# Performance work log

Measured on AMD Instinct MI355X. Metric: run time of the kernel, lower is better.

Reference implementation:

```python
import jax, jax.numpy as jnp
import numpy as np

B, N, C = 8192, 4, 1024
H = 16
D = C // H              # head_dim = 64
P = 4                   # proj_dim (Linformer reduced length)
IDX_I, IDX_J = 1, 2     # Return_attn_way(use_cls=True, attn_selet_way=0)
SCALE = D ** -0.5


def setup_inputs() -> dict:
    key = jax.random.key(0)
    ks = jax.random.split(key, 6)
    std = 0.02
    x = jax.random.normal(ks[0], (B, N, C), dtype=jnp.float32)
    W_qkv = jax.random.normal(ks[1], (C, 3 * C), dtype=jnp.float32) * std   # qkv_bias=False
    W_proj = jax.random.normal(ks[2], (C, C), dtype=jnp.float32) * std
    b_proj = jnp.zeros((C,), dtype=jnp.float32)
    W_E = jax.random.normal(ks[3], (P, N), dtype=jnp.float32) * std         # torch Linear weight [out,in]
    W_F = jax.random.normal(ks[4], (P, N), dtype=jnp.float32) * std
    return {"x": x, "W_qkv": W_qkv, "W_proj": W_proj, "b_proj": b_proj,
            "W_E": W_E, "W_F": W_F}


def reference(x, W_qkv, W_proj, b_proj, W_E, W_F):
    b, n, c = x.shape
    # qkv projection -> [B,N,3,H,D] -> q,k,v each [B,H,N,D]
    qkv = (x @ W_qkv).reshape(b, n, 3, H, D)
    qkv = jnp.transpose(qkv, (2, 0, 3, 1, 4))
    q, k, v = qkv[0], qkv[1], qkv[2]
    q = q * SCALE  # q_norm/k_norm are Identity (qk_norm=False)

    # gathered single-token score: q[:,:,IDX_I,:] @ k[:,:,IDX_J,:].T -> [B,H,H]
    # (torch transpose(-2,-1) on the [B,H,D] slice swaps H and D)
    attn_sel = jnp.einsum('bhd,bgd->bhg', q[:, :, IDX_I, :], k[:, :, IDX_J, :])
    attn_sel_sig = jax.nn.sigmoid(attn_sel)

    # Linformer E/F projection along the sequence axis: [B,H,N,D] -> [B,H,P,D]
    k_low = jnp.einsum('bhnd,pn->bhpd', k, W_E)
    v_low = jnp.einsum('bhnd,pn->bhpd', v, W_F)

    # reduced softmax attention: [B,H,N,P]
    attn = jnp.einsum('bhnd,bhpd->bhnp', q, k_low)
    attn = jax.nn.softmax(attn, axis=-1)  # attn_drop is identity (p=0, eval)
    out = jnp.einsum('bhnp,bhpd->bhnd', attn, v_low)

    # merge heads and output projection
    out = jnp.transpose(out, (0, 2, 1, 3)).reshape(b, n, c)
    out = out @ W_proj.T + b_proj  # proj_drop identity
    return (out, attn_sel_sig)
```

## Files before the change

kernel.cpp:

```cpp
#include <hip/hip_runtime.h>
#include <hip/hip_bf16.h>

#define B_   8192
#define C_   1024
#define H_   16
#define M_   (B_ * 4)
#define K_   1024
#define N1_  3072

typedef __attribute__((ext_vector_type(8))) short short8;
typedef __attribute__((ext_vector_type(4))) float f32x4;
typedef __attribute__((ext_vector_type(8))) int   int8v;

__device__ __forceinline__ unsigned short f2bf(float f) {
  union { float f; unsigned u; } v; v.f = f;
  unsigned r = v.u + 0x7fffu + ((v.u >> 16) & 1u);
  return (unsigned short)(r >> 16);
}
__device__ __forceinline__ float bf2f(unsigned short u) {
  union { unsigned u; float f; } v; v.u = ((unsigned)u) << 16;
  return v.f;
}
__device__ __forceinline__ int pk_fp8(float a, float b, float c, float d) {
  int r = __builtin_amdgcn_cvt_pk_fp8_f32(a, b, 0, false);
  r = __builtin_amdgcn_cvt_pk_fp8_f32(c, d, r, true);
  return r;
}

__global__ __launch_bounds__(256) void cast_x_k(const float* __restrict__ x,
                                                unsigned char* __restrict__ x8,
                                                unsigned short* __restrict__ xsel) {
  const int row = blockIdx.x;
  const int tid = threadIdx.x;
  float4 v = ((const float4*)(x + (size_t)row * 1024))[tid];
  ((int*)(x8 + (size_t)row * 1024))[tid] = pk_fp8(v.x, v.y, v.z, v.w);
  const int n = row & 3;
  if (n == 1 || n == 2) {
    ushort4 o;
    o.x = f2bf(v.x); o.y = f2bf(v.y); o.z = f2bf(v.z); o.w = f2bf(v.w);
    ((ushort4*)(xsel + ((size_t)(n - 1) * 8192 + (row >> 2)) * 1024))[tid] = o;
  }
}

__global__ __launch_bounds__(256) void transpose_wqkv_k(const float* __restrict__ in,
                                                        unsigned short* __restrict__ outb,
                                                        unsigned char* __restrict__ out8) {
  __shared__ float t[32][33];
  int tx = threadIdx.x, ty = threadIdx.y;
  int j0 = blockIdx.x * 32, c0 = blockIdx.y * 32;
#pragma unroll
  for (int i = 0; i < 4; ++i)
    t[ty + i * 8][tx] = in[(size_t)(c0 + ty + i * 8) * N1_ + j0 + tx];
  __syncthreads();
#pragma unroll
  for (int i = 0; i < 4; ++i) {
    int j = j0 + ty + i * 8;
    float v = t[tx][ty + i * 8];
    if (j < 1024) v *= 0.125f;
    outb[(size_t)j * K_ + c0 + tx] = f2bf(v);
    out8[(size_t)j * K_ + c0 + tx] =
        (unsigned char)(__builtin_amdgcn_cvt_pk_fp8_f32(v * 32.f, v * 32.f, 0, false) & 0xff);
  }
}

__global__ __launch_bounds__(256) void cast_wproj_k(const float* __restrict__ in,
                                                    unsigned char* __restrict__ out) {
  int i = blockIdx.x * 256 + threadIdx.x;
  float4 v = ((const float4*)in)[i];
  ((int*)out)[i] = pk_fp8(v.x * 32.f, v.y * 32.f, v.z * 32.f, v.w * 32.f);
}

__global__ __launch_bounds__(256) void gemm_fixup(const unsigned short* __restrict__ A,
                                                  const unsigned short* __restrict__ B0,
                                                  unsigned short* __restrict__ Cbf) {
  __shared__ unsigned short lsA[128 * 32];
  __shared__ unsigned short lsB[128 * 32];
  const int K = 1024, Ncols = 1024;
  const int tid = threadIdx.x;
  const int wave = tid >> 6, lane = tid & 63;
  const int wm = (wave >> 1) * 64, wn = (wave & 1) * 64;
  const long tile_m = (long)blockIdx.y * 128, tile_n = (long)blockIdx.x * 128;
  const unsigned short* Bm = B0 + (tile_m >= 8192 ? (size_t)1024 * 1024 : 0);

  f32x4 acc[4][4] = {};
  const int ci0 = (wave * 2 + 0) * 64 + lane;
  const int ci1 = (wave * 2 + 1) * 64 + lane;
  const int r0 = ci0 >> 2, kc0 = (ci0 & 3) * 8;
  const int r1 = ci1 >> 2, kc1 = (ci1 & 3) * 8;
  const unsigned short* gA0 = A + (tile_m + r0) * K + kc0;
  const unsigned short* gA1 = A + (tile_m + r1) * K + kc1;
  const unsigned short* gB0 = Bm + (tile_n + r0) * K + kc0;
  const unsigned short* gB1 = Bm + (tile_n + r1) * K + kc1;
  unsigned short* dA0 = lsA + (wave * 2 + 0) * 512;
  unsigned short* dA1 = lsA + (wave * 2 + 1) * 512;
  unsigned short* dB0 = lsB + (wave * 2 + 0) * 512;
  unsigned short* dB1 = lsB + (wave * 2 + 1) * 512;
  const int r16 = lane & 15, q8 = (lane >> 4) * 8;

  for (int kt = 0; kt < K; kt += 32) {
    __builtin_amdgcn_global_load_lds((const __attribute__((address_space(1))) void*)(gA0 + kt),
                                     (__attribute__((address_space(3))) void*)dA0, 16, 0, 0);
    __builtin_amdgcn_global_load_lds((const __attribute__((address_space(1))) void*)(gA1 + kt),
                                     (__attribute__((address_space(3))) void*)dA1, 16, 0, 0);
    __builtin_amdgcn_global_load_lds((const __attribute__((address_space(1))) void*)(gB0 + kt),
                                     (__attribute__((address_space(3))) void*)dB0, 16, 0, 0);
    __builtin_amdgcn_global_load_lds((const __attribute__((address_space(1))) void*)(gB1 + kt),
                                     (__attribute__((address_space(3))) void*)dB1, 16, 0, 0);
    __syncthreads();
    short8 afr[4], bfr[4];
#pragma unroll
    for (int mi = 0; mi < 4; ++mi)
      afr[mi] = *(const short8*)&lsA[(wm + mi * 16 + r16) * 32 + q8];
#pragma unroll
    for (int ni = 0; ni < 4; ++ni)
      bfr[ni] = *(const short8*)&lsB[(wn + ni * 16 + r16) * 32 + q8];
#pragma unroll
    for (int mi = 0; mi < 4; ++mi)
#pragma unroll
      for (int ni = 0; ni < 4; ++ni)
        acc[mi][ni] = __builtin_amdgcn_mfma_f32_16x16x32_bf16(afr[mi], bfr[ni], acc[mi][ni], 0, 0, 0);
    __syncthreads();
  }
  const int cl = lane & 15, rq = (lane >> 4) * 4;
#pragma unroll
  for (int mi = 0; mi < 4; ++mi)
#pragma unroll
    for (int ni = 0; ni < 4; ++ni) {
      long col = tile_n + wn + ni * 16 + cl;
#pragma unroll
      for (int r = 0; r < 4; ++r) {
        long row = tile_m + wm + mi * 16 + rq + r;
        Cbf[(size_t)row * Ncols + col] = f2bf(acc[mi][ni][r]);
      }
    }
}

template <int OUTMODE>
__global__ __launch_bounds__(512) void gemm_mx(const unsigned char* __restrict__ A,
                                               const unsigned char* __restrict__ Bm,
                                               unsigned short* __restrict__ Cbf,
                                               float* __restrict__ Cf,
                                               const float* __restrict__ bias,
                                               int K, int Ncols, int sA, int sB) {
  __shared__ unsigned char lds[131072];
  unsigned char* lsA0 = lds;
  unsigned char* lsB0 = lds + 32768;
  unsigned char* lsA1 = lds + 65536;
  unsigned char* lsB1 = lds + 98304;

  const int tid = threadIdx.x;
  const int wave = tid >> 6, lane = tid & 63;
  const int wm = (wave >> 2) * 128;
  const int wn = (wave & 3) * 64;
  const long tile_m = (long)blockIdx.y * 256, tile_n = (long)blockIdx.x * 256;

  f32x4 acc[8][4] = {};

  unsigned offA[4], offB[4];
#pragma unroll
  for (int j = 0; j < 4; ++j) {
    int ci = j * 512 + tid;
    int blk = ci >> 10, idb = ci & 1023;
    int qg = idb >> 8, id = idb & 255;
    int r2 = (id >> 3) & 1, r3 = (id >> 4) & 1;
    int rr0 = ((id >> 1) & 1) ^ r2, rr1 = ((id >> 2) & 1) ^ r3;
    int row = rr0 | (rr1 << 1) | (r2 << 2) | (r3 << 3) | ((id >> 5) << 4);
    int half = (id & 1) ^ rr0;
    offA[j] = (unsigned)((tile_m + blk * 128 + row) * K + qg * 32 + half * 16);
    offB[j] = (unsigned)((tile_n + blk * 128 + row) * K + qg * 32 + half * 16);
  }

  auto stage = [&](int kt, unsigned char* lA, unsigned char* lB) {
#pragma unroll
    for (int j = 0; j < 4; ++j)
      __builtin_amdgcn_global_load_lds(
          (const __attribute__((address_space(1))) void*)(A + offA[j] + kt),
          (__attribute__((address_space(3))) void*)(lA + j * 8192 + wave * 1024), 16, 0, 0);
#pragma unroll
    for (int j = 0; j < 4; ++j)
      __builtin_amdgcn_global_load_lds(
          (const __attribute__((address_space(1))) void*)(Bm + offB[j] + kt),
          (__attribute__((address_space(3))) void*)(lB + j * 8192 + wave * 1024), 16, 0, 0);
  };

  const int hl = lane & 15, qg = lane >> 4;
  const int swz = (hl & 12) << 3;
  const int laneFragBase = qg * 4096 + ((hl * 32) ^ swz) + ((hl & 1) << 4);
  const int Abase = (wm >> 7) * 16384 + laneFragBase;
  const int Bbase = (wn >> 7) * 16384 + (wn & 64) * 32 + laneFragBase;

  const int NT = K >> 7;
  stage(0, lsA0, lsB0);
  stage(128, lsA1, lsB1);
  asm volatile("s_waitcnt vmcnt(8)" ::: "memory");
  __builtin_amdgcn_s_barrier();

  for (int t = 0; t < NT; ++t) {
    unsigned char* lA = (t & 1) ? lsA1 : lsA0;
    unsigned char* lB = (t & 1) ? lsB1 : lsB0;

    int8v bfr[4];
#pragma unroll
    for (int ni = 0; ni < 4; ++ni) {
      int ad = Bbase + ni * 512;
      int4 h0 = *(const int4*)(lB + ad);
      int4 h1 = *(const int4*)(lB + (ad ^ 16));
      bfr[ni] = int8v{h0.x, h0.y, h0.z, h0.w, h1.x, h1.y, h1.z, h1.w};
    }
#pragma unroll
    for (int p = 0; p < 4; ++p) {
      int8v af[2];
#pragma unroll
      for (int mm = 0; mm < 2; ++mm) {
        int ad = Abase + (p * 2 + mm) * 512;
        int4 h0 = *(const int4*)(lA + ad);
        int4 h1 = *(const int4*)(lA + (ad ^ 16));
        af[mm] = int8v{h0.x, h0.y, h0.z, h0.w, h1.x, h1.y, h1.z, h1.w};
      }
      __builtin_amdgcn_s_barrier();
      asm volatile("s_waitcnt lgkmcnt(0)" ::: "memory");
      __builtin_amdgcn_s_setprio(1);
#pragma unroll
      for (int mm = 0; mm < 2; ++mm)
#pragma unroll
        for (int ni = 0; ni < 4; ++ni)
          acc[p * 2 + mm][ni] = __builtin_amdgcn_mfma_scale_f32_16x16x128_f8f6f4(
              af[mm], bfr[ni], acc[p * 2 + mm][ni], 0, 0, 0, sA, 0, sB);
      __builtin_amdgcn_s_setprio(0);
      __builtin_amdgcn_s_barrier();
    }
    if (t + 2 < NT) {
      stage((t + 2) << 7, lA, lB);
      asm volatile("s_waitcnt vmcnt(8)" ::: "memory");
      __builtin_amdgcn_s_barrier();
    } else if (t + 1 < NT) {
      asm volatile("s_waitcnt vmcnt(0)" ::: "memory");
      __builtin_amdgcn_s_barrier();
    }
  }

  const int cl = lane & 15, rq = (lane >> 4) * 4;
#pragma unroll
  for (int mi = 0; mi < 8; ++mi)
#pragma unroll
    for (int ni = 0; ni < 4; ++ni) {
      long col = tile_n + wn + ni * 16 + cl;
      float bv = (OUTMODE == 1) ? bias[col] : 0.f;
#pragma unroll
      for (int r = 0; r < 4; ++r) {
        long row = tile_m + wm + mi * 16 + rq + r;
        if (OUTMODE == 0)
          Cbf[(size_t)row * Ncols + col] = f2bf(acc[mi][ni][r]);
        else
          Cf[(size_t)row * Ncols + col] = acc[mi][ni][r] + bv;
      }
    }
}

__global__ __launch_bounds__(256) void attn_mfma_k(const unsigned short* __restrict__ qkv,
                                                   const unsigned short* __restrict__ q1,
                                                   const unsigned short* __restrict__ k2,
                                                   const float* __restrict__ WE,
                                                   const float* __restrict__ WF,
                                                   unsigned char* __restrict__ hmid8,
                                                   float* __restrict__ attn_sel) {
  __shared__ float As[4][16 * 17 + 2];
  const int tid = threadIdx.x;
  const int wave = tid >> 6, lane = tid & 63;
  const int b = blockIdx.x * 4 + wave;
  const size_t qb = (size_t)b * 4 * N1_;
  const int hl = lane & 15, qg = lane >> 4;

  f32x4 accS[4][4] = {};
  f32x4 accSel = {};
#pragma unroll
  for (int ch = 0; ch < 2; ++ch) {
    const int off = ch * 32 + qg * 8;
    short8 qf[4], kf[4];
#pragma unroll
    for (int n = 0; n < 4; ++n)
      qf[n] = *(const short8*)(qkv + qb + (size_t)n * N1_ + 0 + hl * 64 + off);
#pragma unroll
    for (int m = 0; m < 4; ++m)
      kf[m] = *(const short8*)(qkv + qb + (size_t)m * N1_ + 1024 + hl * 64 + off);
#pragma unroll
    for (int n = 0; n < 4; ++n)
#pragma unroll
      for (int m = 0; m < 4; ++m)
        accS[n][m] = __builtin_amdgcn_mfma_f32_16x16x32_bf16(qf[n], kf[m], accS[n][m], 0, 0, 0);
    short8 qs = *(const short8*)(q1 + (size_t)b * 1024 + hl * 64 + off);
    short8 ks = *(const short8*)(k2 + (size_t)b * 1024 + hl * 64 + off);
    accSel = __builtin_amdgcn_mfma_f32_16x16x32_bf16(qs, ks, accSel, 0, 0, 0);
  }

#pragma unroll
  for (int r = 0; r < 4; ++r)
    attn_sel[(size_t)b * 256 + (qg * 4 + r) * 16 + hl] = 1.f / (1.f + __expf(-accSel[r]));

  if ((hl >> 2) == qg) {
    const int h = hl, rr = h & 3;
    float Sm[4][4];
#pragma unroll
    for (int n = 0; n < 4; ++n)
#pragma unroll
      for (int m = 0; m < 4; ++m) Sm[n][m] = accS[n][m][rr];
#pragma unroll
    for (int n = 0; n < 4; ++n) {
      float lg[4];
#pragma unroll
      for (int p = 0; p < 4; ++p)
        lg[p] = Sm[n][0] * WE[p * 4] + Sm[n][1] * WE[p * 4 + 1] +
                Sm[n][2] * WE[p * 4 + 2] + Sm[n][3] * WE[p * 4 + 3];
      float mx = fmaxf(fmaxf(lg[0], lg[1]), fmaxf(lg[2], lg[3]));
      float e0 = __expf(lg[0] - mx), e1 = __expf(lg[1] - mx);
      float e2 = __expf(lg[2] - mx), e3 = __expf(lg[3] - mx);
      float inv = 1.f / (e0 + e1 + e2 + e3);
      e0 *= inv; e1 *= inv; e2 *= inv; e3 *= inv;
#pragma unroll
      for (int m = 0; m < 4; ++m)
        As[wave][h * 17 + n * 4 + m] =
            e0 * WF[0 * 4 + m] + e1 * WF[1 * 4 + m] + e2 * WF[2 * 4 + m] + e3 * WF[3 * 4 + m];
    }
  }
  __syncthreads();

  {
    const int h = lane & 15, dg = lane >> 4;
    float Ap[4][4];
#pragma unroll
    for (int n = 0; n < 4; ++n)
#pragma unroll
      for (int m = 0; m < 4; ++m) Ap[n][m] = As[wave][h * 17 + n * 4 + m];

    float outv[4][16] = {};
#pragma unroll
    for (int m = 0; m < 4; ++m) {
      const unsigned short* vp = qkv + qb + (size_t)m * N1_ + 2048 + h * 64 + dg * 16;
      short8 v0 = *(const short8*)(vp);
      short8 v1 = *(const short8*)(vp + 8);
      float vf[16];
#pragma unroll
      for (int j = 0; j < 8; ++j) {
        vf[j] = bf2f((unsigned short)v0[j]);
        vf[8 + j] = bf2f((unsigned short)v1[j]);
      }
#pragma unroll
      for (int n = 0; n < 4; ++n)
#pragma unroll
        for (int d = 0; d < 16; ++d) outv[n][d] += Ap[n][m] * vf[d];
    }
#pragma unroll
    for (int n = 0; n < 4; ++n) {
      int w0 = pk_fp8(outv[n][0] * 32.f, outv[n][1] * 32.f, outv[n][2] * 32.f, outv[n][3] * 32.f);
      int w1 = pk_fp8(outv[n][4] * 32.f, outv[n][5] * 32.f, outv[n][6] * 32.f, outv[n][7] * 32.f);
      int w2 = pk_fp8(outv[n][8] * 32.f, outv[n][9] * 32.f, outv[n][10] * 32.f, outv[n][11] * 32.f);
      int w3 = pk_fp8(outv[n][12] * 32.f, outv[n][13] * 32.f, outv[n][14] * 32.f, outv[n][15] * 32.f);
      *(int4*)(hmid8 + ((size_t)b * 4 + n) * 1024 + h * 64 + dg * 16) = make_int4(w0, w1, w2, w3);
    }
  }
}

extern "C" void kernel_launch(void* const* d_in, const int* in_sizes, int n_in,
                              void* d_out, int out_size, void* d_ws, size_t ws_size,
                              hipStream_t stream) {
  (void)in_sizes; (void)n_in; (void)out_size; (void)ws_size;
  const float* x      = (const float*)d_in[0];
  const float* W_qkv  = (const float*)d_in[1];
  const float* W_proj = (const float*)d_in[2];
  const float* b_proj = (const float*)d_in[3];
  const float* W_E    = (const float*)d_in[4];
  const float* W_F    = (const float*)d_in[5];

  float* out0 = (float*)d_out;
  float* out1 = out0 + (size_t)M_ * C_;

  char* ws = (char*)d_ws;
  unsigned short* xsel   = (unsigned short*)(ws);
  unsigned short* wqkvTb = (unsigned short*)(ws + 33554432);
  unsigned short* qkv_bf = (unsigned short*)(ws);
  unsigned char*  x8     = (unsigned char*)(ws + 201326592);
  unsigned char*  hmid8  = x8;
  unsigned char*  wqkvT8 = (unsigned char*)(ws + 234881024);
  unsigned char*  wproj8 = (unsigned char*)(ws + 238026752);
  unsigned short* q1k2   = (unsigned short*)(ws + 239075328);

  cast_x_k<<<32768, 256, 0, stream>>>(x, x8, xsel);
  transpose_wqkv_k<<<dim3(96, 32), dim3(32, 8), 0, stream>>>(W_qkv, wqkvTb, wqkvT8);
  cast_wproj_k<<<1024, 256, 0, stream>>>(W_proj, wproj8);

  gemm_fixup<<<dim3(8, 128), 256, 0, stream>>>(xsel, wqkvTb, q1k2);

  gemm_mx<0><<<dim3(12, 128), 512, 0, stream>>>(x8, wqkvT8, qkv_bf, nullptr, nullptr,
                                                1024, 3072, 127, 122);

  attn_mfma_k<<<B_ / 4, 256, 0, stream>>>(qkv_bf, q1k2, q1k2 + (size_t)8192 * 1024,
                                          W_E, W_F, hmid8, out1);

  gemm_mx<1><<<dim3(4, 128), 512, 0, stream>>>(hmid8, wproj8, nullptr, out0, b_proj,
                                               1024, 1024, 122, 122);
}
```

Baseline: 599.9 us.

## Restructure MX GEMM main loop with split prefetch and fewer barriers

Result: faster. 556.6 us (-7.2%).

```diff
diff --git a/kernel.cpp b/kernel.cpp
--- a/kernel.cpp
+++ b/kernel.cpp
@@ -143,10 +143,6 @@
                                                const float* __restrict__ bias,
                                                int K, int Ncols, int sA, int sB) {
   __shared__ unsigned char lds[131072];
-  unsigned char* lsA0 = lds;
-  unsigned char* lsB0 = lds + 32768;
-  unsigned char* lsA1 = lds + 65536;
-  unsigned char* lsB1 = lds + 98304;
 
   const int tid = threadIdx.x;
   const int wave = tid >> 6, lane = tid & 63;
@@ -170,73 +166,93 @@
     offB[j] = (unsigned)((tile_n + blk * 128 + row) * K + qg * 32 + half * 16);
   }
 
-  auto stage = [&](int kt, unsigned char* lA, unsigned char* lB) {
-#pragma unroll
-    for (int j = 0; j < 4; ++j)
-      __builtin_amdgcn_global_load_lds(
-          (const __attribute__((address_space(1))) void*)(A + offA[j] + kt),
-          (__attribute__((address_space(3))) void*)(lA + j * 8192 + wave * 1024), 16, 0, 0);
-#pragma unroll
-    for (int j = 0; j < 4; ++j)
-      __builtin_amdgcn_global_load_lds(
-          (const __attribute__((address_space(1))) void*)(Bm + offB[j] + kt),
-          (__attribute__((address_space(3))) void*)(lB + j * 8192 + wave * 1024), 16, 0, 0);
-  };
-
   const int hl = lane & 15, qg = lane >> 4;
   const int swz = (hl & 12) << 3;
   const int laneFragBase = qg * 4096 + ((hl * 32) ^ swz) + ((hl & 1) << 4);
   const int Abase = (wm >> 7) * 16384 + laneFragBase;
   const int Bbase = (wn >> 7) * 16384 + (wn & 64) * 32 + laneFragBase;
 
+  auto stage_pair = [&](int kt, unsigned char* dA, unsigned char* dB, int j) {
+    __builtin_amdgcn_global_load_lds(
+        (const __attribute__((address_space(1))) void*)(A + offA[j] + kt),
+        (__attribute__((address_space(3))) void*)(dA + j * 8192 + wave * 1024), 16, 0, 0);
+    __builtin_amdgcn_global_load_lds(
+        (const __attribute__((address_space(1))) void*)(Bm + offB[j] + kt),
+        (__attribute__((address_space(3))) void*)(dB + j * 8192 + wave * 1024), 16, 0, 0);
+  };
+
   const int NT = K >> 7;
-  stage(0, lsA0, lsB0);
-  stage(128, lsA1, lsB1);
-  asm volatile("s_waitcnt vmcnt(8)" ::: "memory");
-  __builtin_amdgcn_s_barrier();
+  stage_pair(0, lds, lds + 32768, 0);
+  stage_pair(0, lds, lds + 32768, 1);
+  stage_pair(0, lds, lds + 32768, 2);
+  stage_pair(0, lds, lds + 32768, 3);
 
   for (int t = 0; t < NT; ++t) {
-    unsigned char* lA = (t & 1) ? lsA1 : lsA0;
-    unsigned char* lB = (t & 1) ? lsB1 : lsB0;
+    unsigned char* bA = lds + (t & 1) * 65536;
+    unsigned char* bB = bA + 32768;
+    unsigned char* nA = lds + ((t + 1) & 1) * 65536;
+    unsigned char* nB = nA + 32768;
+    const int ktn = (t + 1) << 7;
+
+    if (t + 1 < NT) {
+      stage_pair(ktn, nA, nB, 0);
+      stage_pair(ktn, nA, nB, 1);
+      asm volatile("s_waitcnt vmcnt(4)" ::: "memory");
+    } else {
+      asm volatile("s_waitcnt vmcnt(0)" ::: "memory");
+    }
+    __builtin_amdgcn_s_barrier();
 
     int8v bfr[4];
 #pragma unroll
     for (int ni = 0; ni < 4; ++ni) {
       int ad = Bbase + ni * 512;
-      int4 h0 = *(const int4*)(lB + ad);
-      int4 h1 = *(const int4*)(lB + (ad ^ 16));
+      int4 h0 = *(const int4*)(bB + ad);
+      int4 h1 = *(const int4*)(bB + (ad ^ 16));
       bfr[ni] = int8v{h0.x, h0.y, h0.z, h0.w, h1.x, h1.y, h1.z, h1.w};
     }
-#pragma unroll
-    for (int p = 0; p < 4; ++p) {
-      int8v af[2];
-#pragma unroll
-      for (int mm = 0; mm < 2; ++mm) {
-        int ad = Abase + (p * 2 + mm) * 512;
-        int4 h0 = *(const int4*)(lA + ad);
-        int4 h1 = *(const int4*)(lA + (ad ^ 16));
-        af[mm] = int8v{h0.x, h0.y, h0.z, h0.w, h1.x, h1.y, h1.z, h1.w};
+    {
+      int8v af[4];
+#pragma unroll
+      for (int mi = 0; mi < 4; ++mi) {
+        int ad = Abase + mi * 512;
+        int4 h0 = *(const int4*)(bA + ad);
+        int4 h1 = *(const int4*)(bA + (ad ^ 16));
+        af[mi] = int8v{h0.x, h0.y, h0.z, h0.w, h1.x, h1.y, h1.z, h1.w};
       }
-      __builtin_amdgcn_s_barrier();
-      asm volatile("s_waitcnt lgkmcnt(0)" ::: "memory");
       __builtin_amdgcn_s_setprio(1);
 #pragma unroll
-      for (int mm = 0; mm < 2; ++mm)
+      for (int mi = 0; mi < 4; ++mi)
 #pragma unroll
         for (int ni = 0; ni < 4; ++ni)
-          acc[p * 2 + mm][ni] = __builtin_amdgcn_mfma_scale_f32_16x16x128_f8f6f4(
-              af[mm], bfr[ni], acc[p * 2 + mm][ni], 0, 0, 0, sA, 0, sB);
+          acc[mi][ni] = __builtin_amdgcn_mfma_scale_f32_16x16x128_f8f6f4(
+              af[mi], bfr[ni], acc[mi][ni], 0, 0, 0, sA, 0, sB);
       __builtin_amdgcn_s_setprio(0);
-      __builtin_amdgcn_s_barrier();
-    }
-    if (t + 2 < NT) {
-      stage((t + 2) << 7, lA, lB);
-      asm volatile("s_waitcnt vmcnt(8)" ::: "memory");
-      __builtin_amdgcn_s_barrier();
-    } else if (t + 1 < NT) {
-      asm volatile("s_waitcnt vmcnt(0)" ::: "memory");
-      __builtin_amdgcn_s_barrier();
-    }
+    }
+
+    if (t + 1 < NT) {
+      stage_pair(ktn, nA, nB, 2);
+      stage_pair(ktn, nA, nB, 3);
+    }
+    {
+      int8v af[4];
+#pragma unroll
+      for (int mi = 0; mi < 4; ++mi) {
+        int ad = Abase + (mi + 4) * 512;
+        int4 h0 = *(const int4*)(bA + ad);
+        int4 h1 = *(const int4*)(bA + (ad ^ 16));
+        af[mi] = int8v{h0.x, h0.y, h0.z, h0.w, h1.x, h1.y, h1.z, h1.w};
+      }
+      __builtin_amdgcn_s_setprio(1);
+#pragma unroll
+      for (int mi = 0; mi < 4; ++mi)
+#pragma unroll
+        for (int ni = 0; ni < 4; ++ni)
+          acc[mi + 4][ni] = __builtin_amdgcn_mfma_scale_f32_16x16x128_f8f6f4(
+              af[mi], bfr[ni], acc[mi + 4][ni], 0, 0, 0, sA, 0, sB);
+      __builtin_amdgcn_s_setprio(0);
+    }
+    __builtin_amdgcn_s_barrier();
   }
 
   const int cl = lane & 15, rq = (lane >> 4) * 4;
```
